# Optimization experiments

Measured on AMD Instinct MI355X. Metric: run time of the kernel, lower is better.

The kernel has to match this reference:

```python
import jax, jax.numpy as jnp
import numpy as np

NUM_ITERATIONS = 3
EPS = 1e-8


def squash(s, axis=-1):
    # scale = |s|^2/(1+|s|^2), output = scale * s / (|s| + eps)
    norm = jnp.linalg.norm(s, axis=axis, keepdims=True)
    scale = (norm ** 2) / (1.0 + norm ** 2)
    return scale * s / (norm + EPS)


def setup_inputs() -> dict:
    key = jax.random.key(0)
    k_u, k_w = jax.random.split(key)
    B, N, in_dim = 64, 1024, 64
    E, out_dim = 8, 32
    u = jax.random.normal(k_u, (B, N, in_dim), dtype=jnp.float32)
    W = jax.random.normal(k_w, (N, E, out_dim, in_dim), dtype=jnp.float32)
    return {"u": u, "W": W}


def reference(u, W):
    # u: [B, N, in_dim]; W: [N, E, out_dim, in_dim]
    # u_hat[b,n,e,o] = sum_i W[n,e,o,i] * u[b,n,i]
    u_hat = jnp.einsum('neoi,bni->bneo', W, u)  # [B, N, E, out_dim]
    B, N, E, _ = u_hat.shape
    b = jnp.zeros((B, N, E), dtype=u_hat.dtype)
    v = None
    for r in range(NUM_ITERATIONS):
        c = jax.nn.softmax(b, axis=2)[..., None]          # [B, N, E, 1]
        s = jnp.sum(c * u_hat, axis=1)                     # [B, E, out_dim]
        v = squash(s)                                      # [B, E, out_dim]
        if r < NUM_ITERATIONS - 1:
            uv = jnp.einsum('bneo,beo->bne', u_hat, v)     # agreement
            b = b + uv
    return v
```

## Files before the change

### kernel.cpp

```cpp
#include <hip/hip_runtime.h>


#define B_  64
#define N_  1024
#define I_  64
#define E_  8
#define O_  32
#define EO_ 256
#define PAD_ 72

typedef __bf16 bf16x8 __attribute__((ext_vector_type(8)));
typedef __bf16 bf16x4v __attribute__((ext_vector_type(4)));
typedef float  f32x4  __attribute__((ext_vector_type(4)));

__device__ __forceinline__ float bf2f(unsigned int h) {
    unsigned int x = (h & 0xffffu) << 16;
    return __builtin_bit_cast(float, x);
}
__device__ __forceinline__ void cvt_store4(unsigned short* dst, float4 q) {
    bf16x4v v;
    v[0] = (__bf16)q.x; v[1] = (__bf16)q.y; v[2] = (__bf16)q.z; v[3] = (__bf16)q.w;
    *(bf16x4v*)dst = v;
}
__device__ __forceinline__ bf16x8 cvt8(const float* __restrict__ p) {
    float4 q0 = *(const float4*)p;
    float4 q1 = *(const float4*)(p + 4);
    bf16x8 a;
    a[0] = (__bf16)q0.x; a[1] = (__bf16)q0.y; a[2] = (__bf16)q0.z; a[3] = (__bf16)q0.w;
    a[4] = (__bf16)q1.x; a[5] = (__bf16)q1.y; a[6] = (__bf16)q1.z; a[7] = (__bf16)q1.w;
    return a;
}
__device__ __forceinline__ float4 squash4(float4 s4) {
    float sq = s4.x * s4.x + s4.y * s4.y + s4.z * s4.z + s4.w * s4.w;
    sq += __shfl_xor(sq, 1);
    sq += __shfl_xor(sq, 2);
    sq += __shfl_xor(sq, 4);
    float nrm = sqrtf(sq);
    float sc = sq / ((1.f + sq) * (nrm + 1e-8f));
    return make_float4(sc * s4.x, sc * s4.y, sc * s4.z, sc * s4.w);
}

__global__ __launch_bounds__(256) void k_uhat(const float* __restrict__ u,
                                              const float* __restrict__ W,
                                              unsigned short* __restrict__ uh,
                                              float* __restrict__ s012) {
    const int n = blockIdx.x;
    const int t = threadIdx.x;
    const int w = t >> 6, l = t & 63;
    const int m16 = l & 15, g = l >> 4;

    if (n < 3) {
        float* sz = s012 + n * (B_ * EO_);
#pragma unroll
        for (int i = 0; i < 64; ++i) sz[i * 256 + t] = 0.f;
    }

    __shared__ __align__(16) unsigned short sh[B_ * 264];
    unsigned short* ul = sh;
    unsigned short* Dt = sh;

#pragma unroll
    for (int j = 0; j < 4; ++j) {
        int idx = j * 256 + t;
        int b = idx >> 4, c = idx & 15;
        float4 q = *(const float4*)(u + (size_t)b * (N_ * I_) + n * I_ + c * 4);
        cvt_store4(&ul[b * PAD_ + c * 4], q);
    }
    __syncthreads();

    bf16x8 afr[4][2];
#pragma unroll
    for (int mt = 0; mt < 4; ++mt)
#pragma unroll
        for (int ks = 0; ks < 2; ++ks)
            afr[mt][ks] = *(const bf16x8*)&ul[(mt * 16 + m16) * PAD_ + ks * 32 + g * 8];
    __syncthreads();

    f32x4 acc[4][4];
#pragma unroll
    for (int nt = 0; nt < 4; ++nt)
#pragma unroll
        for (int mt = 0; mt < 4; ++mt)
            acc[nt][mt] = (f32x4){0.f, 0.f, 0.f, 0.f};

    const float* Wn = W + (size_t)n * (EO_ * I_);
#pragma unroll
    for (int nt = 0; nt < 4; ++nt) {
        const int eo = w * 64 + nt * 16 + m16;
        const float* wp = Wn + (size_t)eo * I_ + g * 8;
        bf16x8 b0 = cvt8(wp);
        bf16x8 b1 = cvt8(wp + 32);
#pragma unroll
        for (int mt = 0; mt < 4; ++mt) {
            acc[nt][mt] = __builtin_amdgcn_mfma_f32_16x16x32_bf16(afr[mt][0], b0, acc[nt][mt], 0, 0, 0);
            acc[nt][mt] = __builtin_amdgcn_mfma_f32_16x16x32_bf16(afr[mt][1], b1, acc[nt][mt], 0, 0, 0);
        }
    }

#pragma unroll
    for (int nt = 0; nt < 4; ++nt) {
        const int col = w * 64 + nt * 16 + m16;
#pragma unroll
        for (int mt = 0; mt < 4; ++mt)
#pragma unroll
            for (int r = 0; r < 4; ++r) {
                __bf16 hv = (__bf16)acc[nt][mt][r];
                Dt[(mt * 16 + g * 4 + r) * 264 + col] =
                    __builtin_bit_cast(unsigned short, hv);
            }
    }
    __syncthreads();
#pragma unroll
    for (int r = 0; r < 16; ++r) {
        const int row = r * 4 + w;
        uint2 q = *(const uint2*)&Dt[row * 264 + l * 4];
        *(uint2*)(uh + (size_t)row * (N_ * EO_) + (size_t)n * EO_ + l * 4) = q;
    }
}

__global__ __launch_bounds__(256) void k_route(const unsigned short* __restrict__ uh,
                                               const float* __restrict__ s0,
                                               const float* __restrict__ s1,
                                               float* __restrict__ tgt,
                                               int it) {
    const int blk = blockIdx.x;
    const int b = blk >> 5, chunk = blk & 31;
    const int t = threadIdx.x, wave = t >> 6, l = t & 63;

    const unsigned short* base = uh + (size_t)b * (N_ * EO_)
                                    + (size_t)(chunk * 32 + wave * 8) * EO_ + 4 * l;
    float x[8][4];
    float c[8];

    if (it == 0) {
#pragma unroll
        for (int nn = 0; nn < 8; ++nn) {
            uint2 p = *(const uint2*)(base + nn * EO_);
            x[nn][0] = bf2f(p.x); x[nn][1] = bf2f(p.x >> 16);
            x[nn][2] = bf2f(p.y); x[nn][3] = bf2f(p.y >> 16);
            c[nn] = 0.125f;
        }
    } else {
        float4 v4 = squash4(*(const float4*)(s0 + b * EO_ + 4 * l));
        if (it == 2) {
            float4 v1 = squash4(*(const float4*)(s1 + b * EO_ + 4 * l));
            v4.x += v1.x; v4.y += v1.y; v4.z += v1.z; v4.w += v1.w;
        }
        float lg[8];
#pragma unroll
        for (int nn = 0; nn < 8; ++nn) {
            uint2 p = *(const uint2*)(base + nn * EO_);
            x[nn][0] = bf2f(p.x); x[nn][1] = bf2f(p.x >> 16);
            x[nn][2] = bf2f(p.y); x[nn][3] = bf2f(p.y >> 16);
            float pd = x[nn][0] * v4.x + x[nn][1] * v4.y
                     + x[nn][2] * v4.z + x[nn][3] * v4.w;
            pd += __shfl_xor(pd, 1);
            pd += __shfl_xor(pd, 2);
            pd += __shfl_xor(pd, 4);
            lg[nn] = pd;
        }
        float mx[8];
#pragma unroll
        for (int nn = 0; nn < 8; ++nn) mx[nn] = lg[nn];
#pragma unroll
        for (int nn = 0; nn < 8; ++nn) mx[nn] = fmaxf(mx[nn], __shfl_xor(mx[nn], 8));
#pragma unroll
        for (int nn = 0; nn < 8; ++nn) mx[nn] = fmaxf(mx[nn], __shfl_xor(mx[nn], 16));
#pragma unroll
        for (int nn = 0; nn < 8; ++nn) mx[nn] = fmaxf(mx[nn], __shfl_xor(mx[nn], 32));
        float ex[8], sm[8];
#pragma unroll
        for (int nn = 0; nn < 8; ++nn) { ex[nn] = __expf(lg[nn] - mx[nn]); sm[nn] = ex[nn]; }
#pragma unroll
        for (int nn = 0; nn < 8; ++nn) sm[nn] += __shfl_xor(sm[nn], 8);
#pragma unroll
        for (int nn = 0; nn < 8; ++nn) sm[nn] += __shfl_xor(sm[nn], 16);
#pragma unroll
        for (int nn = 0; nn < 8; ++nn) sm[nn] += __shfl_xor(sm[nn], 32);
#pragma unroll
        for (int nn = 0; nn < 8; ++nn) c[nn] = ex[nn] * __builtin_amdgcn_rcpf(sm[nn]);
    }

    float a0 = 0.f, a1 = 0.f, a2 = 0.f, a3 = 0.f;
#pragma unroll
    for (int nn = 0; nn < 8; ++nn) {
        a0 = fmaf(c[nn], x[nn][0], a0); a1 = fmaf(c[nn], x[nn][1], a1);
        a2 = fmaf(c[nn], x[nn][2], a2); a3 = fmaf(c[nn], x[nn][3], a3);
    }

    __shared__ __align__(16) float red[4][EO_];
    *(float4*)&red[wave][4 * l] = make_float4(a0, a1, a2, a3);
    __syncthreads();
    atomicAdd(&tgt[b * EO_ + t], red[0][t] + red[1][t] + red[2][t] + red[3][t]);
}

__global__ __launch_bounds__(256) void k_out(const float* __restrict__ s2,
                                             float* __restrict__ out) {
    const int b = blockIdx.x, t = threadIdx.x;
    float sv = s2[b * EO_ + t];
    float sq = sv * sv;
    sq += __shfl_xor(sq, 1);
    sq += __shfl_xor(sq, 2);
    sq += __shfl_xor(sq, 4);
    sq += __shfl_xor(sq, 8);
    sq += __shfl_xor(sq, 16);
    float nrm = sqrtf(sq);
    out[b * EO_ + t] = sq / ((1.f + sq) * (nrm + 1e-8f)) * sv;
}

extern "C" void kernel_launch(void* const* d_in, const int* in_sizes, int n_in,
                              void* d_out, int out_size, void* d_ws, size_t ws_size,
                              hipStream_t stream) {
    const float* u = (const float*)d_in[0];
    const float* W = (const float*)d_in[1];
    float* out = (float*)d_out;

    char* ws = (char*)d_ws;
    unsigned short* uh = (unsigned short*)ws;
    float* s0 = (float*)(ws + 33554432);
    float* s1 = (float*)(ws + 33620 * 1024);
    float* s2 = (float*)(ws + 34492416);

    s1 = s0 + B_ * EO_;
    s2 = s1 + B_ * EO_;

    k_uhat <<<dim3(N_),   dim3(256), 0, stream>>>(u, W, uh, s0);
    k_route<<<dim3(2048), dim3(256), 0, stream>>>(uh, s0, s1, s0, 0);
    k_route<<<dim3(2048), dim3(256), 0, stream>>>(uh, s0, s1, s1, 1);
    k_route<<<dim3(2048), dim3(256), 0, stream>>>(uh, s0, s1, s2, 2);
    k_out  <<<dim3(B_),   dim3(256), 0, stream>>>(s2, out);
}
```

Baseline: 134.9 us.

## Store u_hat in MFMA fragment layout and route four batches per block

k_uhat now writes accumulator fragments straight to global memory in an MFMA-native packed layout, which removes the LDS transpose and two barriers and lowers LDS use so more blocks can be resident (launch bounds set to 4). k_route reads that layout with 16-byte loads covering four batch rows per lane and handles 4 batches by 16 capsules per block, halving the grid and spreading atomics over more batches per block. The cost is a more intricate index mapping between the two kernels and more registers per thread in the routing kernel.

Measured after the change: 146.4 us. +8.5%, slower.

```diff
diff --git a/kernel.cpp b/kernel.cpp
--- a/kernel.cpp
+++ b/kernel.cpp
@@ -40,10 +40,10 @@
     return make_float4(sc * s4.x, sc * s4.y, sc * s4.z, sc * s4.w);
 }
 
-__global__ __launch_bounds__(256) void k_uhat(const float* __restrict__ u,
-                                              const float* __restrict__ W,
-                                              unsigned short* __restrict__ uh,
-                                              float* __restrict__ s012) {
+__global__ __launch_bounds__(256, 4) void k_uhat(const float* __restrict__ u,
+                                                 const float* __restrict__ W,
+                                                 uint2* __restrict__ uh,
+                                                 float* __restrict__ s012) {
     const int n = blockIdx.x;
     const int t = threadIdx.x;
     const int w = t >> 6, l = t & 63;
@@ -55,9 +55,7 @@
         for (int i = 0; i < 64; ++i) sz[i * 256 + t] = 0.f;
     }
 
-    __shared__ __align__(16) unsigned short sh[B_ * 264];
-    unsigned short* ul = sh;
-    unsigned short* Dt = sh;
+    __shared__ __align__(16) unsigned short ul[B_ * PAD_];
 
 #pragma unroll
     for (int j = 0; j < 4; ++j) {
@@ -74,7 +72,6 @@
 #pragma unroll
         for (int ks = 0; ks < 2; ++ks)
             afr[mt][ks] = *(const bf16x8*)&ul[(mt * 16 + m16) * PAD_ + ks * 32 + g * 8];
-    __syncthreads();
 
     f32x4 acc[4][4];
 #pragma unroll
@@ -97,101 +94,131 @@
         }
     }
 
-#pragma unroll
-    for (int nt = 0; nt < 4; ++nt) {
-        const int col = w * 64 + nt * 16 + m16;
-#pragma unroll
-        for (int mt = 0; mt < 4; ++mt)
-#pragma unroll
-            for (int r = 0; r < 4; ++r) {
-                __bf16 hv = (__bf16)acc[nt][mt][r];
-                Dt[(mt * 16 + g * 4 + r) * 264 + col] =
-                    __builtin_bit_cast(unsigned short, hv);
-            }
-    }
-    __syncthreads();
-#pragma unroll
-    for (int r = 0; r < 16; ++r) {
-        const int row = r * 4 + w;
-        uint2 q = *(const uint2*)&Dt[row * 264 + l * 4];
-        *(uint2*)(uh + (size_t)row * (N_ * EO_) + (size_t)n * EO_ + l * 4) = q;
-    }
-}
-
-__global__ __launch_bounds__(256) void k_route(const unsigned short* __restrict__ uh,
+    uint2* uhn = uh + (size_t)n * 4096 + w * 1024;
+#pragma unroll
+    for (int nt = 0; nt < 4; ++nt)
+#pragma unroll
+        for (int mt = 0; mt < 4; ++mt) {
+            __bf16 h0 = (__bf16)acc[nt][mt][0];
+            __bf16 h1 = (__bf16)acc[nt][mt][1];
+            __bf16 h2 = (__bf16)acc[nt][mt][2];
+            __bf16 h3 = (__bf16)acc[nt][mt][3];
+            uint2 p;
+            p.x = (unsigned)__builtin_bit_cast(unsigned short, h0)
+                | ((unsigned)__builtin_bit_cast(unsigned short, h1) << 16);
+            p.y = (unsigned)__builtin_bit_cast(unsigned short, h2)
+                | ((unsigned)__builtin_bit_cast(unsigned short, h3) << 16);
+            uhn[nt * 256 + mt * 64 + l] = p;
+        }
+}
+
+__global__ __launch_bounds__(256) void k_route(const uint2* __restrict__ uh,
                                                const float* __restrict__ s0,
                                                const float* __restrict__ s1,
                                                float* __restrict__ tgt,
                                                int it) {
     const int blk = blockIdx.x;
-    const int b = blk >> 5, chunk = blk & 31;
+    const int bg = blk >> 6;
+    const int chunk = blk & 63;
     const int t = threadIdx.x, wave = t >> 6, l = t & 63;
 
-    const unsigned short* base = uh + (size_t)b * (N_ * EO_)
-                                    + (size_t)(chunk * 32 + wave * 8) * EO_ + 4 * l;
-    float x[8][4];
-    float c[8];
-
-    if (it == 0) {
-#pragma unroll
-        for (int nn = 0; nn < 8; ++nn) {
-            uint2 p = *(const uint2*)(base + nn * EO_);
-            x[nn][0] = bf2f(p.x); x[nn][1] = bf2f(p.x >> 16);
-            x[nn][2] = bf2f(p.y); x[nn][3] = bf2f(p.y >> 16);
-            c[nn] = 0.125f;
-        }
-    } else {
-        float4 v4 = squash4(*(const float4*)(s0 + b * EO_ + 4 * l));
-        if (it == 2) {
-            float4 v1 = squash4(*(const float4*)(s1 + b * EO_ + 4 * l));
-            v4.x += v1.x; v4.y += v1.y; v4.z += v1.z; v4.w += v1.w;
-        }
-        float lg[8];
-#pragma unroll
-        for (int nn = 0; nn < 8; ++nn) {
-            uint2 p = *(const uint2*)(base + nn * EO_);
-            x[nn][0] = bf2f(p.x); x[nn][1] = bf2f(p.x >> 16);
-            x[nn][2] = bf2f(p.y); x[nn][3] = bf2f(p.y >> 16);
-            float pd = x[nn][0] * v4.x + x[nn][1] * v4.y
-                     + x[nn][2] * v4.z + x[nn][3] * v4.w;
-            pd += __shfl_xor(pd, 1);
-            pd += __shfl_xor(pd, 2);
-            pd += __shfl_xor(pd, 4);
-            lg[nn] = pd;
-        }
-        float mx[8];
-#pragma unroll
-        for (int nn = 0; nn < 8; ++nn) mx[nn] = lg[nn];
-#pragma unroll
-        for (int nn = 0; nn < 8; ++nn) mx[nn] = fmaxf(mx[nn], __shfl_xor(mx[nn], 8));
-#pragma unroll
-        for (int nn = 0; nn < 8; ++nn) mx[nn] = fmaxf(mx[nn], __shfl_xor(mx[nn], 16));
-#pragma unroll
-        for (int nn = 0; nn < 8; ++nn) mx[nn] = fmaxf(mx[nn], __shfl_xor(mx[nn], 32));
-        float ex[8], sm[8];
-#pragma unroll
-        for (int nn = 0; nn < 8; ++nn) { ex[nn] = __expf(lg[nn] - mx[nn]); sm[nn] = ex[nn]; }
-#pragma unroll
-        for (int nn = 0; nn < 8; ++nn) sm[nn] += __shfl_xor(sm[nn], 8);
-#pragma unroll
-        for (int nn = 0; nn < 8; ++nn) sm[nn] += __shfl_xor(sm[nn], 16);
-#pragma unroll
-        for (int nn = 0; nn < 8; ++nn) sm[nn] += __shfl_xor(sm[nn], 32);
-#pragma unroll
-        for (int nn = 0; nn < 8; ++nn) c[nn] = ex[nn] * __builtin_amdgcn_rcpf(sm[nn]);
-    }
-
-    float a0 = 0.f, a1 = 0.f, a2 = 0.f, a3 = 0.f;
-#pragma unroll
-    for (int nn = 0; nn < 8; ++nn) {
-        a0 = fmaf(c[nn], x[nn][0], a0); a1 = fmaf(c[nn], x[nn][1], a1);
-        a2 = fmaf(c[nn], x[nn][2], a2); a3 = fmaf(c[nn], x[nn][3], a3);
-    }
-
-    __shared__ __align__(16) float red[4][EO_];
-    *(float4*)&red[wave][4 * l] = make_float4(a0, a1, a2, a3);
+    const int laneoff = ((l >> 4) * 1024 + ((l >> 2) & 3) * 256 + bg * 16 + (l & 3) * 4) >> 1;
+    const uint4* base = (const uint4*)uh;
+    const int n0 = chunk * 16 + wave * 4;
+
+    float4 vv[4];
+    if (it != 0) {
+#pragma unroll
+        for (int r = 0; r < 4; ++r) {
+            const int b = bg * 4 + r;
+            float4 v4 = squash4(*(const float4*)(s0 + b * EO_ + 4 * l));
+            if (it == 2) {
+                float4 v1 = squash4(*(const float4*)(s1 + b * EO_ + 4 * l));
+                v4.x += v1.x; v4.y += v1.y; v4.z += v1.z; v4.w += v1.w;
+            }
+            vv[r] = v4;
+        }
+    }
+
+    uint4 LA[4][2];
+#pragma unroll
+    for (int nn = 0; nn < 4; ++nn) {
+        const size_t nb = (size_t)(n0 + nn) * 2048 + laneoff;
+        LA[nn][0] = base[nb];
+        LA[nn][1] = base[nb + 1];
+    }
+
+    float acc[4][4];
+#pragma unroll
+    for (int r = 0; r < 4; ++r)
+#pragma unroll
+        for (int q = 0; q < 4; ++q) acc[r][q] = 0.f;
+
+#pragma unroll
+    for (int nn = 0; nn < 4; ++nn) {
+        const uint4 L0 = LA[nn][0], L1 = LA[nn][1];
+        float x[4][4];
+        x[0][0] = bf2f(L0.x); x[1][0] = bf2f(L0.x >> 16);
+        x[2][0] = bf2f(L0.y); x[3][0] = bf2f(L0.y >> 16);
+        x[0][1] = bf2f(L0.z); x[1][1] = bf2f(L0.z >> 16);
+        x[2][1] = bf2f(L0.w); x[3][1] = bf2f(L0.w >> 16);
+        x[0][2] = bf2f(L1.x); x[1][2] = bf2f(L1.x >> 16);
+        x[2][2] = bf2f(L1.y); x[3][2] = bf2f(L1.y >> 16);
+        x[0][3] = bf2f(L1.z); x[1][3] = bf2f(L1.z >> 16);
+        x[2][3] = bf2f(L1.w); x[3][3] = bf2f(L1.w >> 16);
+
+        float c[4];
+        if (it == 0) {
+            c[0] = c[1] = c[2] = c[3] = 0.125f;
+        } else {
+            float lg[4];
+#pragma unroll
+            for (int r = 0; r < 4; ++r) {
+                float pd = x[r][0] * vv[r].x + x[r][1] * vv[r].y
+                         + x[r][2] * vv[r].z + x[r][3] * vv[r].w;
+                pd += __shfl_xor(pd, 1);
+                pd += __shfl_xor(pd, 2);
+                pd += __shfl_xor(pd, 4);
+                lg[r] = pd;
+            }
+            float mx[4];
+#pragma unroll
+            for (int r = 0; r < 4; ++r) mx[r] = lg[r];
+#pragma unroll
+            for (int r = 0; r < 4; ++r) mx[r] = fmaxf(mx[r], __shfl_xor(mx[r], 8));
+#pragma unroll
+            for (int r = 0; r < 4; ++r) mx[r] = fmaxf(mx[r], __shfl_xor(mx[r], 16));
+#pragma unroll
+            for (int r = 0; r < 4; ++r) mx[r] = fmaxf(mx[r], __shfl_xor(mx[r], 32));
+            float ex[4], sm[4];
+#pragma unroll
+            for (int r = 0; r < 4; ++r) { ex[r] = __expf(lg[r] - mx[r]); sm[r] = ex[r]; }
+#pragma unroll
+            for (int r = 0; r < 4; ++r) sm[r] += __shfl_xor(sm[r], 8);
+#pragma unroll
+            for (int r = 0; r < 4; ++r) sm[r] += __shfl_xor(sm[r], 16);
+#pragma unroll
+            for (int r = 0; r < 4; ++r) sm[r] += __shfl_xor(sm[r], 32);
+#pragma unroll
+            for (int r = 0; r < 4; ++r) c[r] = ex[r] * __builtin_amdgcn_rcpf(sm[r]);
+        }
+#pragma unroll
+        for (int r = 0; r < 4; ++r)
+#pragma unroll
+            for (int q = 0; q < 4; ++q)
+                acc[r][q] = fmaf(c[r], x[r][q], acc[r][q]);
+    }
+
+    __shared__ __align__(16) float red[4][4][EO_];
+#pragma unroll
+    for (int r = 0; r < 4; ++r)
+        *(float4*)&red[wave][r][4 * l] = make_float4(acc[r][0], acc[r][1], acc[r][2], acc[r][3]);
     __syncthreads();
-    atomicAdd(&tgt[b * EO_ + t], red[0][t] + red[1][t] + red[2][t] + red[3][t]);
+#pragma unroll
+    for (int r = 0; r < 4; ++r) {
+        float v = red[0][r][t] + red[1][r][t] + red[2][r][t] + red[3][r][t];
+        atomicAdd(&tgt[(bg * 4 + r) * EO_ + t], v);
+    }
 }
 
 __global__ __launch_bounds__(256) void k_out(const float* __restrict__ s2,
@@ -216,17 +243,14 @@
     float* out = (float*)d_out;
 
     char* ws = (char*)d_ws;
-    unsigned short* uh = (unsigned short*)ws;
+    uint2* uh = (uint2*)ws;
     float* s0 = (float*)(ws + 33554432);
-    float* s1 = (float*)(ws + 33620 * 1024);
-    float* s2 = (float*)(ws + 34492416);
-
-    s1 = s0 + B_ * EO_;
-    s2 = s1 + B_ * EO_;
+    float* s1 = s0 + B_ * EO_;
+    float* s2 = s1 + B_ * EO_;
 
     k_uhat <<<dim3(N_),   dim3(256), 0, stream>>>(u, W, uh, s0);
-    k_route<<<dim3(2048), dim3(256), 0, stream>>>(uh, s0, s1, s0, 0);
-    k_route<<<dim3(2048), dim3(256), 0, stream>>>(uh, s0, s1, s1, 1);
-    k_route<<<dim3(2048), dim3(256), 0, stream>>>(uh, s0, s1, s2, 2);
+    k_route<<<dim3(1024), dim3(256), 0, stream>>>(uh, s0, s1, s0, 0);
+    k_route<<<dim3(1024), dim3(256), 0, stream>>>(uh, s0, s1, s1, 1);
+    k_route<<<dim3(1024), dim3(256), 0, stream>>>(uh, s0, s1, s2, 2);
     k_out  <<<dim3(B_),   dim3(256), 0, stream>>>(s2, out);
 }
```

## Fuse routing iterations and output squash into one per-batch kernel

Applied to the files above, without the earlier changes.

Replaces the three atomic-accumulating routing launches and the final squash kernel with one kernel that assigns a block per batch and loops over all routing iterations internally. The squashed v is kept in shared memory, which removes the global atomics, the zeroing of the partial sums and the extra launches. In exchange, the grid shrinks to 64 blocks, which leaves most compute units idle and makes each block stream its whole u_hat slice serially.

After: 183.9 us. 1.36x slower.

```diff
diff --git a/kernel.cpp b/kernel.cpp
--- a/kernel.cpp
+++ b/kernel.cpp
@@ -30,30 +30,14 @@
     a[4] = (__bf16)q1.x; a[5] = (__bf16)q1.y; a[6] = (__bf16)q1.z; a[7] = (__bf16)q1.w;
     return a;
 }
-__device__ __forceinline__ float4 squash4(float4 s4) {
-    float sq = s4.x * s4.x + s4.y * s4.y + s4.z * s4.z + s4.w * s4.w;
-    sq += __shfl_xor(sq, 1);
-    sq += __shfl_xor(sq, 2);
-    sq += __shfl_xor(sq, 4);
-    float nrm = sqrtf(sq);
-    float sc = sq / ((1.f + sq) * (nrm + 1e-8f));
-    return make_float4(sc * s4.x, sc * s4.y, sc * s4.z, sc * s4.w);
-}
 
 __global__ __launch_bounds__(256) void k_uhat(const float* __restrict__ u,
                                               const float* __restrict__ W,
-                                              unsigned short* __restrict__ uh,
-                                              float* __restrict__ s012) {
+                                              unsigned short* __restrict__ uh) {
     const int n = blockIdx.x;
     const int t = threadIdx.x;
     const int w = t >> 6, l = t & 63;
     const int m16 = l & 15, g = l >> 4;
-
-    if (n < 3) {
-        float* sz = s012 + n * (B_ * EO_);
-#pragma unroll
-        for (int i = 0; i < 64; ++i) sz[i * 256 + t] = 0.f;
-    }
 
     __shared__ __align__(16) unsigned short sh[B_ * 264];
     unsigned short* ul = sh;
@@ -118,94 +102,95 @@
     }
 }
 
-__global__ __launch_bounds__(256) void k_route(const unsigned short* __restrict__ uh,
-                                               const float* __restrict__ s0,
-                                               const float* __restrict__ s1,
-                                               float* __restrict__ tgt,
-                                               int it) {
-    const int blk = blockIdx.x;
-    const int b = blk >> 5, chunk = blk & 31;
-    const int t = threadIdx.x, wave = t >> 6, l = t & 63;
-
-    const unsigned short* base = uh + (size_t)b * (N_ * EO_)
-                                    + (size_t)(chunk * 32 + wave * 8) * EO_ + 4 * l;
-    float x[8][4];
-    float c[8];
-
-    if (it == 0) {
-#pragma unroll
-        for (int nn = 0; nn < 8; ++nn) {
-            uint2 p = *(const uint2*)(base + nn * EO_);
-            x[nn][0] = bf2f(p.x); x[nn][1] = bf2f(p.x >> 16);
-            x[nn][2] = bf2f(p.y); x[nn][3] = bf2f(p.y >> 16);
-            c[nn] = 0.125f;
+__global__ __launch_bounds__(512) void k_route_all(const unsigned short* __restrict__ uh,
+                                                   float* __restrict__ out) {
+    const int b = blockIdx.x;
+    const int t = threadIdx.x;
+    const int wave = t >> 6, l = t & 63;
+
+    const unsigned short* ub = uh + (size_t)b * (N_ * EO_) + 4 * l;
+
+    __shared__ __align__(16) float red[8][EO_];
+    __shared__ __align__(16) float vcur[EO_];
+
+    for (int it = 0; it < 3; ++it) {
+        float4 vv;
+        if (it != 0) vv = *(const float4*)&vcur[4 * l];
+
+        float a0 = 0.f, a1 = 0.f, a2 = 0.f, a3 = 0.f;
+
+        for (int pass = 0; pass < 16; ++pass) {
+            const unsigned short* base = ub + (size_t)(pass * 64 + wave * 8) * EO_;
+            float x[8][4];
+            float c[8];
+#pragma unroll
+            for (int nn = 0; nn < 8; ++nn) {
+                uint2 p = *(const uint2*)(base + nn * EO_);
+                x[nn][0] = bf2f(p.x); x[nn][1] = bf2f(p.x >> 16);
+                x[nn][2] = bf2f(p.y); x[nn][3] = bf2f(p.y >> 16);
+            }
+            if (it == 0) {
+#pragma unroll
+                for (int nn = 0; nn < 8; ++nn) c[nn] = 0.125f;
+            } else {
+                float lg[8];
+#pragma unroll
+                for (int nn = 0; nn < 8; ++nn) {
+                    float pd = x[nn][0] * vv.x + x[nn][1] * vv.y
+                             + x[nn][2] * vv.z + x[nn][3] * vv.w;
+                    pd += __shfl_xor(pd, 1);
+                    pd += __shfl_xor(pd, 2);
+                    pd += __shfl_xor(pd, 4);
+                    lg[nn] = pd;
+                }
+                float mx[8];
+#pragma unroll
+                for (int nn = 0; nn < 8; ++nn) mx[nn] = lg[nn];
+#pragma unroll
+                for (int nn = 0; nn < 8; ++nn) mx[nn] = fmaxf(mx[nn], __shfl_xor(mx[nn], 8));
+#pragma unroll
+                for (int nn = 0; nn < 8; ++nn) mx[nn] = fmaxf(mx[nn], __shfl_xor(mx[nn], 16));
+#pragma unroll
+                for (int nn = 0; nn < 8; ++nn) mx[nn] = fmaxf(mx[nn], __shfl_xor(mx[nn], 32));
+                float ex[8], sm[8];
+#pragma unroll
+                for (int nn = 0; nn < 8; ++nn) { ex[nn] = __expf(lg[nn] - mx[nn]); sm[nn] = ex[nn]; }
+#pragma unroll
+                for (int nn = 0; nn < 8; ++nn) sm[nn] += __shfl_xor(sm[nn], 8);
+#pragma unroll
+                for (int nn = 0; nn < 8; ++nn) sm[nn] += __shfl_xor(sm[nn], 16);
+#pragma unroll
+                for (int nn = 0; nn < 8; ++nn) sm[nn] += __shfl_xor(sm[nn], 32);
+#pragma unroll
+                for (int nn = 0; nn < 8; ++nn) c[nn] = ex[nn] * __builtin_amdgcn_rcpf(sm[nn]);
+            }
+#pragma unroll
+            for (int nn = 0; nn < 8; ++nn) {
+                a0 = fmaf(c[nn], x[nn][0], a0); a1 = fmaf(c[nn], x[nn][1], a1);
+                a2 = fmaf(c[nn], x[nn][2], a2); a3 = fmaf(c[nn], x[nn][3], a3);
+            }
         }
-    } else {
-        float4 v4 = squash4(*(const float4*)(s0 + b * EO_ + 4 * l));
-        if (it == 2) {
-            float4 v1 = squash4(*(const float4*)(s1 + b * EO_ + 4 * l));
-            v4.x += v1.x; v4.y += v1.y; v4.z += v1.z; v4.w += v1.w;
+
+        *(float4*)&red[wave][4 * l] = make_float4(a0, a1, a2, a3);
+        __syncthreads();
+
+        if (t < EO_) {
+            float sv = ((red[0][t] + red[1][t]) + (red[2][t] + red[3][t]))
+                     + ((red[4][t] + red[5][t]) + (red[6][t] + red[7][t]));
+            float sq = sv * sv;
+            sq += __shfl_xor(sq, 1);
+            sq += __shfl_xor(sq, 2);
+            sq += __shfl_xor(sq, 4);
+            sq += __shfl_xor(sq, 8);
+            sq += __shfl_xor(sq, 16);
+            float nrm = sqrtf(sq);
+            float vt = sq / ((1.f + sq) * (nrm + 1e-8f)) * sv;
+            if (it == 0)      vcur[t] = vt;
+            else if (it == 1) vcur[t] = vcur[t] + vt;
+            else              out[b * EO_ + t] = vt;
         }
-        float lg[8];
-#pragma unroll
-        for (int nn = 0; nn < 8; ++nn) {
-            uint2 p = *(const uint2*)(base + nn * EO_);
-            x[nn][0] = bf2f(p.x); x[nn][1] = bf2f(p.x >> 16);
-            x[nn][2] = bf2f(p.y); x[nn][3] = bf2f(p.y >> 16);
-            float pd = x[nn][0] * v4.x + x[nn][1] * v4.y
-                     + x[nn][2] * v4.z + x[nn][3] * v4.w;
-            pd += __shfl_xor(pd, 1);
-            pd += __shfl_xor(pd, 2);
-            pd += __shfl_xor(pd, 4);
-            lg[nn] = pd;
-        }
-        float mx[8];
-#pragma unroll
-        for (int nn = 0; nn < 8; ++nn) mx[nn] = lg[nn];
-#pragma unroll
-        for (int nn = 0; nn < 8; ++nn) mx[nn] = fmaxf(mx[nn], __shfl_xor(mx[nn], 8));
-#pragma unroll
-        for (int nn = 0; nn < 8; ++nn) mx[nn] = fmaxf(mx[nn], __shfl_xor(mx[nn], 16));
-#pragma unroll
-        for (int nn = 0; nn < 8; ++nn) mx[nn] = fmaxf(mx[nn], __shfl_xor(mx[nn], 32));
-        float ex[8], sm[8];
-#pragma unroll
-        for (int nn = 0; nn < 8; ++nn) { ex[nn] = __expf(lg[nn] - mx[nn]); sm[nn] = ex[nn]; }
-#pragma unroll
-        for (int nn = 0; nn < 8; ++nn) sm[nn] += __shfl_xor(sm[nn], 8);
-#pragma unroll
-        for (int nn = 0; nn < 8; ++nn) sm[nn] += __shfl_xor(sm[nn], 16);
-#pragma unroll
-        for (int nn = 0; nn < 8; ++nn) sm[nn] += __shfl_xor(sm[nn], 32);
-#pragma unroll
-        for (int nn = 0; nn < 8; ++nn) c[nn] = ex[nn] * __builtin_amdgcn_rcpf(sm[nn]);
-    }
-
-    float a0 = 0.f, a1 = 0.f, a2 = 0.f, a3 = 0.f;
-#pragma unroll
-    for (int nn = 0; nn < 8; ++nn) {
-        a0 = fmaf(c[nn], x[nn][0], a0); a1 = fmaf(c[nn], x[nn][1], a1);
-        a2 = fmaf(c[nn], x[nn][2], a2); a3 = fmaf(c[nn], x[nn][3], a3);
-    }
-
-    __shared__ __align__(16) float red[4][EO_];
-    *(float4*)&red[wave][4 * l] = make_float4(a0, a1, a2, a3);
-    __syncthreads();
-    atomicAdd(&tgt[b * EO_ + t], red[0][t] + red[1][t] + red[2][t] + red[3][t]);
-}
-
-__global__ __launch_bounds__(256) void k_out(const float* __restrict__ s2,
-                                             float* __restrict__ out) {
-    const int b = blockIdx.x, t = threadIdx.x;
-    float sv = s2[b * EO_ + t];
-    float sq = sv * sv;
-    sq += __shfl_xor(sq, 1);
-    sq += __shfl_xor(sq, 2);
-    sq += __shfl_xor(sq, 4);
-    sq += __shfl_xor(sq, 8);
-    sq += __shfl_xor(sq, 16);
-    float nrm = sqrtf(sq);
-    out[b * EO_ + t] = sq / ((1.f + sq) * (nrm + 1e-8f)) * sv;
+        __syncthreads();
+    }
 }
 
 extern "C" void kernel_launch(void* const* d_in, const int* in_sizes, int n_in,
@@ -215,18 +200,8 @@
     const float* W = (const float*)d_in[1];
     float* out = (float*)d_out;
 
-    char* ws = (char*)d_ws;
-    unsigned short* uh = (unsigned short*)ws;
-    float* s0 = (float*)(ws + 33554432);
-    float* s1 = (float*)(ws + 33620 * 1024);
-    float* s2 = (float*)(ws + 34492416);
-
-    s1 = s0 + B_ * EO_;
-    s2 = s1 + B_ * EO_;
-
-    k_uhat <<<dim3(N_),   dim3(256), 0, stream>>>(u, W, uh, s0);
-    k_route<<<dim3(2048), dim3(256), 0, stream>>>(uh, s0, s1, s0, 0);
-    k_route<<<dim3(2048), dim3(256), 0, stream>>>(uh, s0, s1, s1, 1);
-    k_route<<<dim3(2048), dim3(256), 0, stream>>>(uh, s0, s1, s2, 2);
-    k_out  <<<dim3(B_),   dim3(256), 0, stream>>>(s2, out);
-}
+    unsigned short* uh = (unsigned short*)d_ws;
+
+    k_uhat     <<<dim3(N_), dim3(256), 0, stream>>>(u, W, uh);
+    k_route_all<<<dim3(B_), dim3(512), 0, stream>>>(uh, out);
+}
```
